# Performance work log

Hardware: AMD Instinct MI355X
Metric: run time of the kernel (lower is better)

Reference implementation:

```python
import jax, jax.numpy as jnp
import numpy as np
import math

B, T, C = 4, 1024, 1024
H = 16          # n_head
E = 8           # num_experts
K = 2           # top_k
HID = 4096      # expert_hidden_dim
TEMP = 1.0
EPS_LN = 1e-5


def setup_inputs() -> dict:
    key = jax.random.key(0)
    ks = jax.random.split(key, 16)
    s = 0.02
    return {
        'x': jax.random.normal(ks[0], (B, T, C), jnp.float32),
        'ln1_g': jnp.ones((C,), jnp.float32),
        'ln1_b': jnp.zeros((C,), jnp.float32),
        'W_qkv': jax.random.normal(ks[1], (C, 3 * C), jnp.float32) * s,
        'b_qkv': jnp.zeros((3 * C,), jnp.float32),
        'W_proj': jax.random.normal(ks[2], (C, C), jnp.float32) * s,
        'b_proj': jnp.zeros((C,), jnp.float32),
        'ln2_g': jnp.ones((C,), jnp.float32),
        'ln2_b': jnp.zeros((C,), jnp.float32),
        'W_router': jax.random.normal(ks[3], (C, E), jnp.float32) * s,
        'W1': jax.random.normal(ks[4], (E, C, HID), jnp.float32) * s,
        'b1': jnp.zeros((E, HID), jnp.float32),
        'W2': jax.random.normal(ks[5], (E, HID, C), jnp.float32) * s,
        'b2': jnp.zeros((E, C), jnp.float32),
    }


def _layernorm(x, g, b):
    mu = jnp.mean(x, axis=-1, keepdims=True)
    var = jnp.mean(jnp.square(x - mu), axis=-1, keepdims=True)
    return (x - mu) * jax.lax.rsqrt(var + EPS_LN) * g + b


def reference(x, ln1_g, ln1_b, W_qkv, b_qkv, W_proj, b_proj,
              ln2_g, ln2_b, W_router, W1, b1, W2, b2):
    D = C // H
    # --- causal self-attention on ln_1(x) ---
    h = _layernorm(x, ln1_g, ln1_b)
    qkv = h @ W_qkv + b_qkv                      # [B,T,3C]
    q, k, v = jnp.split(qkv, 3, axis=-1)
    q = q.reshape(B, T, H, D).transpose(0, 2, 1, 3)   # [B,H,T,D]
    k = k.reshape(B, T, H, D).transpose(0, 2, 1, 3)
    v = v.reshape(B, T, H, D).transpose(0, 2, 1, 3)
    att = jnp.einsum('bhqd,bhkd->bhqk', q, k) * (1.0 / math.sqrt(D))
    mask = jnp.tril(jnp.ones((T, T), bool))
    att = jnp.where(mask, att, -jnp.inf)
    att = jax.nn.softmax(att, axis=-1)
    y = jnp.einsum('bhqk,bhkd->bhqd', att, v)
    y = y.transpose(0, 2, 1, 3).reshape(B, T, C)
    x = x + (y @ W_proj + b_proj)

    # --- sparse MoE on ln_2(x) ---
    h2 = _layernorm(x, ln2_g, ln2_b)
    xf = h2.reshape(-1, C)                       # [N,C]
    N = xf.shape[0]
    logits = (xf @ W_router) / TEMP              # [N,E]
    prob = jax.nn.softmax(logits, axis=-1)
    top_prob, top_idx = jax.lax.top_k(prob, K)   # [N,K]
    top_prob = top_prob / (jnp.sum(top_prob, axis=-1, keepdims=True) + 1e-9)
    # dense per-token per-expert combine weights (0 for unselected experts)
    w = jnp.zeros((N, E), xf.dtype).at[jnp.arange(N)[:, None], top_idx].add(top_prob)
    # dense expert compute (weights zero out unselected experts -> same math)
    hid = jax.nn.gelu(jnp.einsum('nc,ech->neh', xf, W1) + b1, approximate=False)
    eo = jnp.einsum('neh,ehc->nec', hid, W2) + b2          # [N,E,C]
    out_flat = jnp.einsum('nec,ne->nc', eo, w)
    x = x + out_flat.reshape(B, T, C)

    counts = jnp.zeros((E,), jnp.float32).at[top_idx.reshape(-1)].add(1.0)
    expert_utilization = counts / (jnp.sum(counts) + 1e-9)
    return x, expert_utilization
```

## Files before the change

### kernel.cpp

```cpp
#include <hip/hip_runtime.h>
#include <cmath>

#define CDIM 1024
#define NTOK 4096
#define NHEAD 16
#define HDIM 64
#define NEXP 8
#define HIDD 4096
#define MAXROWS 9216

typedef short bf16x8 __attribute__((ext_vector_type(8)));
typedef short s16x4  __attribute__((ext_vector_type(4)));
typedef float f32x4  __attribute__((ext_vector_type(4)));

static __device__ __forceinline__ short f2bf(float f){
  unsigned u = __builtin_bit_cast(unsigned, f);
  u += 0x7fffu + ((u >> 16) & 1u);
  return (short)(u >> 16);
}

static __device__ __forceinline__ int swz64(int r, int ch){
  return r*64 + (((ch ^ (r>>1)) & 3) << 4);
}
static __device__ __forceinline__ int swz128(int r, int ch){
  return r*128 + (((ch ^ r) & 7) << 4);
}

static __device__ __forceinline__ void gl16(const short* g, short* l){
  __builtin_amdgcn_global_load_lds(
      (const __attribute__((address_space(1))) void*)g,
      (__attribute__((address_space(3))) void*)l, 16, 0, 0);
}

__global__ void k_transpose_cast(const float* __restrict__ in, short* __restrict__ out,
                                 int R, int Cc){
  __shared__ float tile[64][65];
  const int z = blockIdx.z;
  const float* src = in + (long long)z*R*Cc;
  short* dst = out + (long long)z*R*Cc;
  const int r0 = blockIdx.y*64, c0 = blockIdx.x*64;
  const int t = threadIdx.x;
  #pragma unroll
  for (int it=0; it<4; ++it){
    const int item = t + it*256;
    const int r = item>>4, c4 = item&15;
    const float4 v = *(const float4*)(src + (long long)(r0+r)*Cc + c0 + c4*4);
    tile[r][c4*4+0]=v.x; tile[r][c4*4+1]=v.y; tile[r][c4*4+2]=v.z; tile[r][c4*4+3]=v.w;
  }
  __syncthreads();
  #pragma unroll
  for (int it=0; it<2; ++it){
    const int item = t + it*256;
    const int rr8 = item & 7, cc = item >> 3;
    bf16x8 o;
    #pragma unroll
    for (int i=0;i<8;i++) o[i] = f2bf(tile[rr8*8+i][cc]);
    *(bf16x8*)(dst + (long long)(c0+cc)*R + r0 + rr8*8) = o;
  }
}

__global__ void k_ln1(const float* __restrict__ x, const float* __restrict__ g,
                      const float* __restrict__ b, short* __restrict__ out){
  const int row = blockIdx.x;
  const int t = threadIdx.x;
  const float4 v = ((const float4*)(x + (long long)row*CDIM))[t];
  float s  = v.x+v.y+v.z+v.w;
  float s2 = v.x*v.x+v.y*v.y+v.z*v.z+v.w*v.w;
  #pragma unroll
  for (int mm=1; mm<64; mm<<=1){ s += __shfl_xor(s,mm); s2 += __shfl_xor(s2,mm); }
  __shared__ float ps[4], ps2[4];
  const int w = t>>6, l = t&63;
  if (l==0){ ps[w]=s; ps2[w]=s2; }
  __syncthreads();
  s  = ps[0]+ps[1]+ps[2]+ps[3];
  s2 = ps2[0]+ps2[1]+ps2[2]+ps2[3];
  const float mu = s*(1.f/CDIM);
  const float rstd = rsqrtf(s2*(1.f/CDIM) - mu*mu + 1e-5f);
  const float4 gg = ((const float4*)g)[t];
  const float4 bb = ((const float4*)b)[t];
  s16x4 o;
  o[0]=f2bf((v.x-mu)*rstd*gg.x+bb.x); o[1]=f2bf((v.y-mu)*rstd*gg.y+bb.y);
  o[2]=f2bf((v.z-mu)*rstd*gg.z+bb.z); o[3]=f2bf((v.w-mu)*rstd*gg.w+bb.w);
  *(s16x4*)(out + (long long)row*CDIM + t*4) = o;
}

__global__ void k_ln2_router(const float* __restrict__ x1, const float* __restrict__ g,
                             const float* __restrict__ b, const float* __restrict__ Wr,
                             short* __restrict__ h2, int* __restrict__ tidx,
                             float* __restrict__ tw, int* __restrict__ counts){
  const int row = blockIdx.x;
  const int t = threadIdx.x;
  const float4 v = ((const float4*)(x1 + (long long)row*CDIM))[t];
  float s  = v.x+v.y+v.z+v.w;
  float s2 = v.x*v.x+v.y*v.y+v.z*v.z+v.w*v.w;
  #pragma unroll
  for (int mm=1; mm<64; mm<<=1){ s += __shfl_xor(s,mm); s2 += __shfl_xor(s2,mm); }
  __shared__ float ps[4], ps2[4];
  const int w = t>>6, l = t&63;
  if (l==0){ ps[w]=s; ps2[w]=s2; }
  __syncthreads();
  s  = ps[0]+ps[1]+ps[2]+ps[3];
  s2 = ps2[0]+ps2[1]+ps2[2]+ps2[3];
  const float mu = s*(1.f/CDIM);
  const float rstd = rsqrtf(s2*(1.f/CDIM) - mu*mu + 1e-5f);
  const float4 gg = ((const float4*)g)[t];
  const float4 bb = ((const float4*)b)[t];
  const float y0=(v.x-mu)*rstd*gg.x+bb.x, y1=(v.y-mu)*rstd*gg.y+bb.y;
  const float y2=(v.z-mu)*rstd*gg.z+bb.z, y3=(v.w-mu)*rstd*gg.w+bb.w;
  s16x4 o; o[0]=f2bf(y0); o[1]=f2bf(y1); o[2]=f2bf(y2); o[3]=f2bf(y3);
  *(s16x4*)(h2 + (long long)row*CDIM + t*4) = o;

  float acc[8];
  const float* wr0 = Wr + (long long)(t*4)*NEXP;
  #pragma unroll
  for (int e=0;e<8;e++) acc[e] = y0*wr0[e] + y1*wr0[8+e] + y2*wr0[16+e] + y3*wr0[24+e];
  #pragma unroll
  for (int mm=1; mm<64; mm<<=1){
    #pragma unroll
    for (int e=0;e<8;e++) acc[e] += __shfl_xor(acc[e], mm);
  }
  __shared__ float pl[4][8];
  if (l==0){
    #pragma unroll
    for (int e=0;e<8;e++) pl[w][e]=acc[e];
  }
  __syncthreads();
  if (t==0){
    float lg[8];
    #pragma unroll
    for (int e=0;e<8;e++) lg[e] = pl[0][e]+pl[1][e]+pl[2][e]+pl[3][e];
    float mx = lg[0];
    #pragma unroll
    for (int e=1;e<8;e++) mx = fmaxf(mx, lg[e]);
    float pr[8]; float sum = 0.f;
    #pragma unroll
    for (int e=0;e<8;e++){ pr[e]=expf(lg[e]-mx); sum += pr[e]; }
    int i0 = 0;
    #pragma unroll
    for (int e=1;e<8;e++) if (pr[e] > pr[i0]) i0 = e;
    int i1 = (i0==0) ? 1 : 0;
    #pragma unroll
    for (int e=0;e<8;e++) if (e!=i0 && pr[e] > pr[i1]) i1 = e;
    const float p0 = pr[i0]/sum, p1 = pr[i1]/sum;
    const float dn = p0 + p1 + 1e-9f;
    tidx[row*2]=i0; tidx[row*2+1]=i1;
    tw[row*2]=p0/dn; tw[row*2+1]=p1/dn;
    atomicAdd(&counts[i0],1); atomicAdd(&counts[i1],1);
  }
}

__global__ void k_route_setup(const int* __restrict__ counts, int* __restrict__ offs,
                              int* __restrict__ cursors, int* __restrict__ rowmap,
                              float* __restrict__ util){
  if (threadIdx.x == 0){
    int o = 0;
    for (int e=0;e<8;e++){
      offs[e] = o; cursors[e] = o;
      o += (counts[e] + 127) & ~127;
    }
    offs[8] = o;
    for (int e=0;e<8;e++) util[e] = (float)counts[e] / 8192.0f;
  }
  for (int i = threadIdx.x; i < MAXROWS; i += blockDim.x) rowmap[i] = -1;
}

__global__ void k_scatter(const int* __restrict__ tidx, const float* __restrict__ tw,
                          int* __restrict__ cursors, int* __restrict__ rowmap,
                          float* __restrict__ roww, int* __restrict__ posmap){
  const int i = blockIdx.x*blockDim.x + threadIdx.x;
  if (i >= 2*NTOK) return;
  const int e = tidx[i];
  const int pos = atomicAdd(&cursors[e], 1);
  rowmap[pos] = i >> 1;
  roww[pos]   = tw[i];
  posmap[i]   = pos;
}

template<int EPI>
__launch_bounds__(512, 4)
__global__ void k_gemm(const short* __restrict__ A, const short* __restrict__ Bt,
                       const float* __restrict__ bias, const float* __restrict__ resid,
                       void* __restrict__ Cout, int N, int K,
                       const int* __restrict__ rowmap, const int* __restrict__ offs,
                       long long expStrideB, const short* __restrict__ zrow){
  int wg = blockIdx.x;
  const int nwg = gridDim.x;
  {
    const int q = nwg >> 3, r8 = nwg & 7;
    const int xcd = wg & 7, pos = wg >> 3;
    wg = (xcd < r8 ? xcd*(q+1) : r8*(q+1) + (xcd - r8)*q) + pos;
  }
  const int gridN = N >> 7;
  const int gridM = nwg / gridN;
  const int mtile = wg % gridM, ntile = wg / gridM;
  const int mbase = mtile*128;
  const int nbase = ntile*128;
  int e = 0;
  if constexpr (EPI >= 2){
    if (mbase >= offs[8]) return;
    while (e < 7 && mbase >= offs[e+1]) e++;
    Bt += (long long)e * expStrideB;
  }
  __shared__ short Asm[2][4096];
  __shared__ short Bsm[2][4096];
  const int tid = threadIdx.x;
  const int w = tid >> 6, l = tid & 63;
  const int wr = w >> 1, wc = w & 1;
  const int l15 = l & 15, l4 = l >> 4;

  const short* aSrc; const short* bSrc;
  {
    const int r = tid >> 2, ch = tid & 3;
    const int sch = (ch ^ (r >> 1)) & 3;
    if constexpr (EPI == 2){
      const int grow = rowmap[mbase + r];
      aSrc = (grow >= 0) ? (A + (long long)grow*K + sch*8) : (zrow + sch*8);
    } else {
      aSrc = A + (long long)(mbase + r)*K + sch*8;
    }
    bSrc = Bt + (long long)(nbase + r)*K + sch*8;
  }
  const int dOff = w*512;

  f32x4 acc[2][4];
  const f32x4 z4 = {0.f,0.f,0.f,0.f};
  #pragma unroll
  for (int i=0;i<2;i++){
    #pragma unroll
    for (int jn=0;jn<4;jn++) acc[i][jn] = z4;
  }

  auto stage = [&](int buf, int kt){
    gl16(aSrc + kt, &Asm[buf][dOff]);
    gl16(bSrc + kt, &Bsm[buf][dOff]);
  };
  auto compute = [&](int buf){
    bf16x8 af[2], bfr[4];
    #pragma unroll
    for (int i=0;i<2;i++)
      af[i]  = *(const bf16x8*)((char*)Asm[buf] + swz64(wr*32 + i*16 + l15, l4));
    #pragma unroll
    for (int jn=0;jn<4;jn++)
      bfr[jn] = *(const bf16x8*)((char*)Bsm[buf] + swz64(wc*64 + jn*16 + l15, l4));
    __builtin_amdgcn_s_setprio(1);
    #pragma unroll
    for (int i=0;i<2;i++){
      #pragma unroll
      for (int jn=0;jn<4;jn++)
        acc[i][jn] = __builtin_amdgcn_mfma_f32_16x16x32_bf16(af[i], bfr[jn], acc[i][jn], 0,0,0);
    }
    __builtin_amdgcn_s_setprio(0);
  };

  stage(0, 0);
  asm volatile("s_waitcnt vmcnt(0)" ::: "memory");
  __builtin_amdgcn_s_barrier();

  int cur = 0;
  for (int kt = 32; kt < K; kt += 32){
    stage(cur ^ 1, kt);
    compute(cur);
    asm volatile("s_waitcnt vmcnt(0)" ::: "memory");
    __builtin_amdgcn_s_barrier();
    cur ^= 1;
  }
  compute(cur);

  #pragma unroll
  for (int i=0;i<2;i++){
    const int row0 = mbase + wr*32 + i*16 + l4*4;
    #pragma unroll
    for (int jn=0;jn<4;jn++){
      const int col = nbase + wc*64 + jn*16 + l15;
      const float bi = bias[(EPI>=2 ? e*N : 0) + col];
      #pragma unroll
      for (int j=0;j<4;j++){
        const long long idx = (long long)(row0 + j)*N + col;
        float v = acc[i][jn][j] + bi;
        if constexpr (EPI == 0){
          ((short*)Cout)[idx] = f2bf(v);
        } else if constexpr (EPI == 1){
          ((float*)Cout)[idx] = v + resid[idx];
        } else if constexpr (EPI == 2){
          ((short*)Cout)[idx] = f2bf(0.5f*v*(1.0f + erff(v*0.70710678118654752f)));
        } else {
          ((float*)Cout)[idx] = v;
        }
      }
    }
  }
}

__launch_bounds__(512)
__global__ void k_attn(const short* __restrict__ qkv, short* __restrict__ y){
  const int qp = blockIdx.x;
  const int bh = blockIdx.y;
  const int bb = bh >> 4;
  const int h  = bh & 15;
  const int tid = threadIdx.x;
  const int w = tid >> 6, l = tid & 63;
  const int half = w >> 2, wq = w & 3;
  const int l15 = l & 15, l4 = l >> 4;

  __shared__ short Ksm[64*64];
  __shared__ short Vtsm[64*64];
  __shared__ short Psm[8*16*64];

  const long long rs = 3*CDIM;
  const int qrow0 = bb*1024 + qp*128;
  const int myQt = (qp << 1) + half;
  const int qtHigh = (qp << 1) + 1;

  bf16x8 aq[2];
  {
    const int qr = qrow0 + half*64 + wq*16 + l15;
    const short* qp2 = qkv + (long long)qr*rs + h*HDIM;
    aq[0] = *(const bf16x8*)(qp2 + l4*8);
    aq[1] = *(const bf16x8*)(qp2 + 32 + l4*8);
  }

  const f32x4 z4 = {0.f,0.f,0.f,0.f};
  f32x4 O[4];
  #pragma unroll
  for (int cf=0;cf<4;cf++) O[cf] = z4;
  float mrow[4], lrow[4];
  #pragma unroll
  for (int j=0;j<4;j++){ mrow[j] = -1e30f; lrow[j] = 0.f; }

  for (int kvb = 0; kvb <= qtHigh; ++kvb){
    const int kvrow0 = bb*1024 + kvb*64;
    {
      const int r = tid >> 3, c = tid & 7;
      const short* kp = qkv + (long long)(kvrow0 + r)*rs + CDIM + h*HDIM + c*8;
      *(bf16x8*)((char*)Ksm + swz128(r, c)) = *(const bf16x8*)kp;
      const short* vp = qkv + (long long)(kvrow0 + r)*rs + 2*CDIM + h*HDIM + c*8;
      bf16x8 vv = *(const bf16x8*)vp;
      const int off2 = 2*r;
      const int g0 = off2 >> 4, b0 = off2 & 15;
      #pragma unroll
      for (int i=0;i<8;i++){
        const int d = c*8 + i;
        *(short*)((char*)Vtsm + d*128 + (((g0 ^ d) & 7) << 4) + b0) = vv[i];
      }
    }
    __syncthreads();

    if (kvb <= myQt){
      f32x4 S[4];
      #pragma unroll
      for (int cf=0;cf<4;cf++) S[cf] = z4;
      #pragma unroll
      for (int cf=0;cf<4;cf++){
        #pragma unroll
        for (int kf=0;kf<2;kf++){
          bf16x8 bk = *(const bf16x8*)((char*)Ksm + swz128(cf*16 + l15, kf*4 + l4));
          S[cf] = __builtin_amdgcn_mfma_f32_16x16x32_bf16(aq[kf], bk, S[cf], 0,0,0);
        }
      }

      const bool diag = (kvb == myQt);
      #pragma unroll
      for (int cf=0;cf<4;cf++){
        #pragma unroll
        for (int j=0;j<4;j++){
          float s = S[cf][j] * 0.125f;
          if (diag && (cf*16 + l15 > wq*16 + l4*4 + j)) s = -1e30f;
          S[cf][j] = s;
        }
      }

      float alpha[4];
      #pragma unroll
      for (int j=0;j<4;j++){
        float mx = fmaxf(fmaxf(S[0][j],S[1][j]), fmaxf(S[2][j],S[3][j]));
        #pragma unroll
        for (int mm=1; mm<16; mm<<=1) mx = fmaxf(mx, __shfl_xor(mx, mm));
        const float mnew = fmaxf(mrow[j], mx);
        const float al = expf(mrow[j] - mnew);
        float psum = 0.f;
        #pragma unroll
        for (int cf=0;cf<4;cf++){ float pp = expf(S[cf][j]-mnew); S[cf][j]=pp; psum += pp; }
        #pragma unroll
        for (int mm=1; mm<16; mm<<=1) psum += __shfl_xor(psum, mm);
        lrow[j] = lrow[j]*al + psum;
        mrow[j] = mnew; alpha[j] = al;
      }
      #pragma unroll
      for (int cf=0;cf<4;cf++){
        #pragma unroll
        for (int j=0;j<4;j++) O[cf][j] *= alpha[j];
      }

      char* pw = (char*)Psm + w*2048;
      #pragma unroll
      for (int cf=0;cf<4;cf++){
        #pragma unroll
        for (int j=0;j<4;j++){
          const int r = l4*4 + j;
          const int cb = (cf*16 + l15)*2;
          *(short*)(pw + r*128 + ((((cb>>4) ^ r) & 7)<<4) + (cb & 15)) = f2bf(S[cf][j]);
        }
      }
      bf16x8 pa[2];
      pa[0] = *(const bf16x8*)(pw + swz128(l15, l4));
      pa[1] = *(const bf16x8*)(pw + swz128(l15, 4 + l4));
      #pragma unroll
      for (int cf=0;cf<4;cf++){
        #pragma unroll
        for (int kf=0;kf<2;kf++){
          bf16x8 bv = *(const bf16x8*)((char*)Vtsm + swz128(cf*16 + l15, kf*4 + l4));
          O[cf] = __builtin_amdgcn_mfma_f32_16x16x32_bf16(pa[kf], bv, O[cf], 0,0,0);
        }
      }
    }
    __syncthreads();
  }

  const int yr0 = qrow0 + half*64 + wq*16;
  #pragma unroll
  for (int cf=0;cf<4;cf++){
    #pragma unroll
    for (int j=0;j<4;j++){
      const int r = l4*4 + j;
      y[(long long)(yr0 + r)*CDIM + h*HDIM + cf*16 + l15] = f2bf(O[cf][j] / lrow[j]);
    }
  }
}

__global__ void k_combine(const float* __restrict__ x1, const float* __restrict__ eo,
                          const int* __restrict__ posmap, const float* __restrict__ roww,
                          float* __restrict__ out){
  const int row = blockIdx.x;
  const int t = threadIdx.x;
  const int p0 = posmap[row*2], p1 = posmap[row*2+1];
  const float w0 = roww[p0], w1 = roww[p1];
  const float4 a  = ((const float4*)(x1 + (long long)row*CDIM))[t];
  const float4 e0 = ((const float4*)(eo + (long long)p0*CDIM))[t];
  const float4 e1 = ((const float4*)(eo + (long long)p1*CDIM))[t];
  float4 r;
  r.x = a.x + w0*e0.x + w1*e1.x;
  r.y = a.y + w0*e0.y + w1*e1.y;
  r.z = a.z + w0*e0.z + w1*e1.z;
  r.w = a.w + w0*e0.w + w1*e1.w;
  ((float4*)(out + (long long)row*CDIM))[t] = r;
}

extern "C" void kernel_launch(void* const* d_in, const int* in_sizes, int n_in,
                              void* d_out, int out_size, void* d_ws, size_t ws_size,
                              hipStream_t stream){
  const float* x     = (const float*)d_in[0];
  const float* ln1_g = (const float*)d_in[1];
  const float* ln1_b = (const float*)d_in[2];
  const float* W_qkv = (const float*)d_in[3];
  const float* b_qkv = (const float*)d_in[4];
  const float* W_proj= (const float*)d_in[5];
  const float* b_proj= (const float*)d_in[6];
  const float* ln2_g = (const float*)d_in[7];
  const float* ln2_b = (const float*)d_in[8];
  const float* W_r   = (const float*)d_in[9];
  const float* W1    = (const float*)d_in[10];
  const float* b1    = (const float*)d_in[11];
  const float* W2    = (const float*)d_in[12];
  const float* b2    = (const float*)d_in[13];
  float* out = (float*)d_out;
  float* util = out + (long long)NTOK*CDIM;

  char* p = (char*)d_ws;
  auto alloc = [&](size_t bytes)->char*{
    char* r = p; p += (bytes + 255) & ~(size_t)255; return r;
  };
  short* Wt1   = (short*)alloc((size_t)NEXP*HIDD*CDIM*2);
  short* Wt2   = (short*)alloc((size_t)NEXP*CDIM*HIDD*2);
  float* x1    = (float*)alloc((size_t)NTOK*CDIM*4);
  short* h2    = (short*)alloc((size_t)NTOK*CDIM*2);
  short* hid   = (short*)alloc((size_t)MAXROWS*HIDD*2);
  int*   tidx  = (int*)alloc(2*NTOK*4);
  float* tw    = (float*)alloc(2*NTOK*4);
  int*   counts= (int*)alloc(256);
  int*   offs  = (int*)alloc(256);
  int*   curs  = (int*)alloc(256);
  int*   rowmap= (int*)alloc(MAXROWS*4);
  float* roww  = (float*)alloc(MAXROWS*4);
  int*   posmap= (int*)alloc(2*NTOK*4);
  short* zrow  = (short*)alloc(8192);
  char* transStart = p;
  short* WtQ = (short*)alloc((size_t)3*CDIM*CDIM*2);
  short* WtP = (short*)alloc((size_t)CDIM*CDIM*2);
  short* h   = (short*)alloc((size_t)NTOK*CDIM*2);
  short* qkv = (short*)alloc((size_t)NTOK*3*CDIM*2);
  short* y   = (short*)alloc((size_t)NTOK*CDIM*2);
  float* eo  = (float*)transStart;

  (void)hipMemsetAsync(counts, 0, 32, stream);
  (void)hipMemsetAsync(zrow, 0, 8192, stream);

  k_transpose_cast<<<dim3(3*CDIM/64, CDIM/64, 1), 256, 0, stream>>>(W_qkv, WtQ, CDIM, 3*CDIM);
  k_transpose_cast<<<dim3(CDIM/64, CDIM/64, 1),   256, 0, stream>>>(W_proj, WtP, CDIM, CDIM);
  k_transpose_cast<<<dim3(HIDD/64, CDIM/64, NEXP),256, 0, stream>>>(W1, Wt1, CDIM, HIDD);
  k_transpose_cast<<<dim3(CDIM/64, HIDD/64, NEXP),256, 0, stream>>>(W2, Wt2, HIDD, CDIM);

  k_ln1<<<NTOK, 256, 0, stream>>>(x, ln1_g, ln1_b, h);

  k_gemm<0><<<dim3((NTOK/128)*(3*CDIM/128)), 512, 0, stream>>>(
      h, WtQ, b_qkv, nullptr, qkv, 3*CDIM, CDIM, nullptr, nullptr, 0, nullptr);

  k_attn<<<dim3(1024/128, 4*NHEAD), 512, 0, stream>>>(qkv, y);

  k_gemm<1><<<dim3((NTOK/128)*(CDIM/128)), 512, 0, stream>>>(
      y, WtP, b_proj, x, x1, CDIM, CDIM, nullptr, nullptr, 0, nullptr);

  k_ln2_router<<<NTOK, 256, 0, stream>>>(x1, ln2_g, ln2_b, W_r, h2, tidx, tw, counts);
  k_route_setup<<<1, 256, 0, stream>>>(counts, offs, curs, rowmap, util);
  k_scatter<<<(2*NTOK)/256, 256, 0, stream>>>(tidx, tw, curs, rowmap, roww, posmap);

  k_gemm<2><<<dim3((MAXROWS/128)*(HIDD/128)), 512, 0, stream>>>(
      h2, Wt1, b1, nullptr, hid, HIDD, CDIM, rowmap, offs, (long long)HIDD*CDIM, zrow);
  k_gemm<3><<<dim3((MAXROWS/128)*(CDIM/128)), 512, 0, stream>>>(
      hid, Wt2, b2, nullptr, eo, CDIM, HIDD, nullptr, offs, (long long)CDIM*HIDD, zrow);

  k_combine<<<NTOK, 256, 0, stream>>>(x1, eo, posmap, roww, out);
}
```

Baseline: 632.9 us.

## Store expert outputs in bf16, drop setprio, memset rowmap via async memset

The second expert GEMM now writes its output as bf16 instead of fp32, and the combine kernel reads and widens those bf16 values. This halves the bytes written and read for expert outputs. The MFMA setprio hints are removed from the GEMM inner loop, and the rowmap -1 fill moves from the single-block setup kernel to a hipMemsetAsync. Rounding the expert outputs to bf16 adds a small precision loss.

Result: no change. 632.0 us (-0.2%).

```diff
diff --git a/kernel.cpp b/kernel.cpp
--- a/kernel.cpp
+++ b/kernel.cpp
@@ -17,6 +17,10 @@
   unsigned u = __builtin_bit_cast(unsigned, f);
   u += 0x7fffu + ((u >> 16) & 1u);
   return (short)(u >> 16);
+}
+static __device__ __forceinline__ float bf2f(short s){
+  unsigned u = ((unsigned)(unsigned short)s) << 16;
+  return __builtin_bit_cast(float, u);
 }
 
 static __device__ __forceinline__ int swz64(int r, int ch){
@@ -150,8 +154,7 @@
 }
 
 __global__ void k_route_setup(const int* __restrict__ counts, int* __restrict__ offs,
-                              int* __restrict__ cursors, int* __restrict__ rowmap,
-                              float* __restrict__ util){
+                              int* __restrict__ cursors, float* __restrict__ util){
   if (threadIdx.x == 0){
     int o = 0;
     for (int e=0;e<8;e++){
@@ -161,7 +164,6 @@
     offs[8] = o;
     for (int e=0;e<8;e++) util[e] = (float)counts[e] / 8192.0f;
   }
-  for (int i = threadIdx.x; i < MAXROWS; i += blockDim.x) rowmap[i] = -1;
 }
 
 __global__ void k_scatter(const int* __restrict__ tidx, const float* __restrict__ tw,
@@ -242,14 +244,12 @@
     #pragma unroll
     for (int jn=0;jn<4;jn++)
       bfr[jn] = *(const bf16x8*)((char*)Bsm[buf] + swz64(wc*64 + jn*16 + l15, l4));
-    __builtin_amdgcn_s_setprio(1);
     #pragma unroll
     for (int i=0;i<2;i++){
       #pragma unroll
       for (int jn=0;jn<4;jn++)
         acc[i][jn] = __builtin_amdgcn_mfma_f32_16x16x32_bf16(af[i], bfr[jn], acc[i][jn], 0,0,0);
     }
-    __builtin_amdgcn_s_setprio(0);
   };
 
   stage(0, 0);
@@ -284,7 +284,7 @@
         } else if constexpr (EPI == 2){
           ((short*)Cout)[idx] = f2bf(0.5f*v*(1.0f + erff(v*0.70710678118654752f)));
         } else {
-          ((float*)Cout)[idx] = v;
+          ((short*)Cout)[idx] = f2bf(v);
         }
       }
     }
@@ -427,7 +427,7 @@
   }
 }
 
-__global__ void k_combine(const float* __restrict__ x1, const float* __restrict__ eo,
+__global__ void k_combine(const float* __restrict__ x1, const short* __restrict__ eo,
                           const int* __restrict__ posmap, const float* __restrict__ roww,
                           float* __restrict__ out){
   const int row = blockIdx.x;
@@ -435,13 +435,13 @@
   const int p0 = posmap[row*2], p1 = posmap[row*2+1];
   const float w0 = roww[p0], w1 = roww[p1];
   const float4 a  = ((const float4*)(x1 + (long long)row*CDIM))[t];
-  const float4 e0 = ((const float4*)(eo + (long long)p0*CDIM))[t];
-  const float4 e1 = ((const float4*)(eo + (long long)p1*CDIM))[t];
+  const s16x4 e0 = *(const s16x4*)(eo + (long long)p0*CDIM + t*4);
+  const s16x4 e1 = *(const s16x4*)(eo + (long long)p1*CDIM + t*4);
   float4 r;
-  r.x = a.x + w0*e0.x + w1*e1.x;
-  r.y = a.y + w0*e0.y + w1*e1.y;
-  r.z = a.z + w0*e0.z + w1*e1.z;
-  r.w = a.w + w0*e0.w + w1*e1.w;
+  r.x = a.x + w0*bf2f(e0[0]) + w1*bf2f(e1[0]);
+  r.y = a.y + w0*bf2f(e0[1]) + w1*bf2f(e1[1]);
+  r.z = a.z + w0*bf2f(e0[2]) + w1*bf2f(e1[2]);
+  r.w = a.w + w0*bf2f(e0[3]) + w1*bf2f(e1[3]);
   ((float4*)(out + (long long)row*CDIM))[t] = r;
 }
 
@@ -489,10 +489,11 @@
   short* h   = (short*)alloc((size_t)NTOK*CDIM*2);
   short* qkv = (short*)alloc((size_t)NTOK*3*CDIM*2);
   short* y   = (short*)alloc((size_t)NTOK*CDIM*2);
-  float* eo  = (float*)transStart;
+  short* eo  = (short*)transStart;
 
   (void)hipMemsetAsync(counts, 0, 32, stream);
   (void)hipMemsetAsync(zrow, 0, 8192, stream);
+  (void)hipMemsetAsync(rowmap, 0xFF, MAXROWS*4, stream);
 
   k_transpose_cast<<<dim3(3*CDIM/64, CDIM/64, 1), 256, 0, stream>>>(W_qkv, WtQ, CDIM, 3*CDIM);
   k_transpose_cast<<<dim3(CDIM/64, CDIM/64, 1),   256, 0, stream>>>(W_proj, WtP, CDIM, CDIM);
@@ -510,7 +511,7 @@
       y, WtP, b_proj, x, x1, CDIM, CDIM, nullptr, nullptr, 0, nullptr);
 
   k_ln2_router<<<NTOK, 256, 0, stream>>>(x1, ln2_g, ln2_b, W_r, h2, tidx, tw, counts);
-  k_route_setup<<<1, 256, 0, stream>>>(counts, offs, curs, rowmap, util);
+  k_route_setup<<<1, 64, 0, stream>>>(counts, offs, curs, util);
   k_scatter<<<(2*NTOK)/256, 256, 0, stream>>>(tidx, tw, curs, rowmap, roww, posmap);
 
   k_gemm<2><<<dim3((MAXROWS/128)*(HIDD/128)), 512, 0, stream>>>(
```
